# Optimization experiments

Measured on AMD Instinct MI355X. Metric: run time of the kernel, lower is better.

## Reference

```python
import jax, jax.numpy as jnp
import numpy as np
from jax import lax

NHEAD = 8
LAYER_POOL = [1, 3, 5]
NUM_KEYS = [2, 2, 2]
N_LAYERS = 6


def ln(x, w, b, eps=1e-5):
    m = x.mean(-1, keepdims=True)
    v = ((x - m) ** 2).mean(-1, keepdims=True)
    return (x - m) / jnp.sqrt(v + eps) * w + b


def separable_attn(x, Wt, bt, Ws, bs_, Wo, bo, B, t, wh, pool_k):
    # x: (L, B, C), L = 1 + t*wh. Separable temporal->spatial attention with
    # std-based temporal token selection (VidTR compact pooling).
    L, _, C = x.shape
    hd = C // NHEAD
    scale = hd ** -0.5
    qkv = x @ Wt + bt                               # (L,B,3C)
    q, k_, v = jnp.split(qkv, 3, axis=-1)
    # --- cls token: full attention over all L tokens ---
    qc = (q[:1] * scale).reshape(1, B, NHEAD, hd)
    kf = k_.reshape(L, B, NHEAD, hd)
    vf = v.reshape(L, B, NHEAD, hd)
    ac = jax.nn.softmax(jnp.einsum('qbhd,lbhd->bhql', qc, kf), axis=-1)
    cls_out = jnp.einsum('bhql,lbhd->qbhd', ac, vf).reshape(1, B, C)
    # --- temporal attention per spatial location ---
    def resh_t(a):
        return a[1:].reshape(t, wh, B, NHEAD, hd).transpose(3, 2, 1, 0, 4)  # (h,B,wh,t,hd)
    qt, kt, vt = resh_t(q) * scale, resh_t(k_), resh_t(v)
    at = jax.nn.softmax(jnp.einsum('hbwqd,hbwkd->hbwqk', qt, kt), axis=-1)  # (h,B,wh,t,t)
    if pool_k > 0:
        sigma = jnp.std(at, axis=-1, ddof=1)        # (h,B,wh,t) row-wise std of attn
        _, idx = lax.top_k(sigma, t - pool_k)        # keep t-k most informative frames
        idx = jnp.sort(idx, axis=-1)                 # restore temporal order
        at = jnp.take_along_axis(at, idx[..., None], axis=3)  # (h,B,wh,t',t)
    else:
        idx = None
    ot = jnp.einsum('hbwqk,hbwkd->hbwqd', at, vt)    # (h,B,wh,t',hd)
    tp = ot.shape[3]
    y = ot.transpose(3, 2, 1, 0, 4).reshape(tp, wh, B, C)
    # --- spatial attention per frame (separate projections) ---
    qkv_s = y @ Ws + bs_
    qs, ks, vs = jnp.split(qkv_s, 3, axis=-1)
    def resh_s(a):
        return a.reshape(tp, wh, B, NHEAD, hd).transpose(3, 2, 0, 1, 4)  # (h,B,t',wh,hd)
    qs, ks, vs = resh_s(qs) * scale, resh_s(ks), resh_s(vs)
    as_ = jax.nn.softmax(jnp.einsum('hbtqd,hbtkd->hbtqk', qs, ks), axis=-1)
    os_ = jnp.einsum('hbtqk,hbtkd->hbtqd', as_, vs)  # (h,B,t',wh,hd)
    y = os_.transpose(2, 3, 1, 0, 4).reshape(tp * wh, B, C)
    out = jnp.concatenate([cls_out, y], axis=0) @ Wo + bo
    return out, idx


def pool_residual(src, idx, B, t, wh):
    # Gather-based temporal pooling of the residual path (the headroom target).
    C = src.shape[-1]
    hd = C // NHEAD
    cls_tok = src[:1]
    twh = src[1:].reshape(t, wh, B, NHEAD, hd).transpose(3, 2, 1, 0, 4)  # (h,B,wh,t,hd)
    twh = jnp.take_along_axis(twh, idx[..., None], axis=3)               # (h,B,wh,t',hd)
    tp = idx.shape[-1]
    twh = twh.transpose(3, 2, 1, 0, 4).reshape(tp * wh, B, C)
    return jnp.concatenate([cls_tok, twh], axis=0)


def setup_inputs() -> dict:
    key = jax.random.key(0)
    ks = jax.random.split(key, 12)
    C, F, ncls, t, P, B = 512, 2048, 157, 16, 16, 8
    def rn(k, shp, s=0.02):
        return jax.random.normal(k, shp, jnp.float32) * s
    return {
        'src': jax.random.normal(ks[0], (B, 3, t, 224, 224), jnp.float32),
        'conv_w': rn(ks[1], (C, 3, 1, P, P)),
        'conv_b': jnp.zeros((C,), jnp.float32),
        'cls_tok': rn(ks[2], (1, 1, C)),
        'pos': rn(ks[3], (1, t * 14 * 14 + 1, C)),
        'Wt': rn(ks[4], (N_LAYERS, C, 3 * C)), 'bt': jnp.zeros((N_LAYERS, 3 * C), jnp.float32),
        'Ws': rn(ks[5], (N_LAYERS, C, 3 * C)), 'bs_': jnp.zeros((N_LAYERS, 3 * C), jnp.float32),
        'Wo': rn(ks[6], (N_LAYERS, C, C)), 'bo': jnp.zeros((N_LAYERS, C), jnp.float32),
        'n1w': jnp.ones((N_LAYERS, C), jnp.float32), 'n1b': jnp.zeros((N_LAYERS, C), jnp.float32),
        'n2w': jnp.ones((N_LAYERS, C), jnp.float32), 'n2b': jnp.zeros((N_LAYERS, C), jnp.float32),
        'W1': rn(ks[7], (N_LAYERS, C, F)), 'b1': jnp.zeros((N_LAYERS, F), jnp.float32),
        'W2': rn(ks[8], (N_LAYERS, F, C)), 'b2': jnp.zeros((N_LAYERS, C), jnp.float32),
        'enw': jnp.ones((C,), jnp.float32), 'enb': jnp.zeros((C,), jnp.float32),
        'fcw': rn(ks[9], (C, ncls)), 'fcb': jnp.zeros((ncls,), jnp.float32),
    }


def reference(src, conv_w, conv_b, cls_tok, pos, Wt, bt, Ws, bs_, Wo, bo,
              n1w, n1b, n2w, n2b, W1, b1, W2, b2, enw, enb, fcw, fcb):
    B = src.shape[0]
    x = lax.conv_general_dilated(src, conv_w, window_strides=(1, 16, 16), padding='VALID',
                                 dimension_numbers=('NCDHW', 'OIDHW', 'NCDHW'))
    x = x + conv_b[None, :, None, None, None]      # (B,C,t,14,14)
    _, C, t, h, w = x.shape
    wh = h * w
    x = x.reshape(B, C, t * wh).transpose(2, 0, 1)  # (t*wh, B, C)
    x = jnp.concatenate([jnp.broadcast_to(cls_tok.transpose(1, 0, 2), (1, B, C)), x], axis=0)
    pos_e = pos.transpose(1, 0, 2)                  # (L,1,C), broadcasts over B
    for i in range(N_LAYERS):
        src2 = ln(x, n1w[i], n1b[i])
        qin = src2 + pos_e if i == 0 else src2
        pk = NUM_KEYS[LAYER_POOL.index(i)] if i in LAYER_POOL else 0
        attn_out, idx = separable_attn(qin, Wt[i], bt[i], Ws[i], bs_[i], Wo[i], bo[i], B, t, wh, pk)
        if i in LAYER_POOL:
            x = pool_residual(x, idx, B, t, wh)
            t = t - pk
        x = x + attn_out
        src2 = ln(x, n2w[i], n2b[i])
        x = x + jax.nn.relu(src2 @ W1[i] + b1[i]) @ W2[i] + b2[i]
    x = ln(x, enw, enb)
    return x[0] @ fcw + fcb                          # (B, activity_num)
```

## Files before the change

### kernel.cpp

```cpp
#include <hip/hip_runtime.h>
#include <math.h>


#define BB 8
#define CC 512
#define HH 8
#define HD 64
#define WHT 196
#define NCLS 157
#define CA_NCH 32

typedef short bf16x8 __attribute__((ext_vector_type(8)));
typedef float floatx4 __attribute__((ext_vector_type(4)));

__device__ __forceinline__ unsigned short f2bf(float f) {
  unsigned u = __float_as_uint(f);
  unsigned r = u + 0x7FFFu + ((u >> 16) & 1u);
  return (unsigned short)(r >> 16);
}
__device__ __forceinline__ float bf2f(unsigned short h) {
  return __uint_as_float((unsigned)h << 16);
}
__device__ __forceinline__ void splitf(float x, unsigned short& h, unsigned short& l) {
  unsigned u = __float_as_uint(x);
  unsigned hs = u >> 16;
  float rem = x - __uint_as_float(hs << 16);
  h = (unsigned short)hs;
  l = f2bf(rem);
}

__device__ __forceinline__ void glds16(const unsigned short* g, unsigned short* l) {
  __builtin_amdgcn_global_load_lds(
      (const __attribute__((address_space(1))) void*)g,
      (__attribute__((address_space(3))) void*)l, 16, 0, 0);
}

__device__ __forceinline__ float wave_reduce_sum(float v) {
#pragma unroll
  for (int o = 32; o > 0; o >>= 1) v += __shfl_down(v, o, 64);
  return v;
}
__device__ __forceinline__ float wave_reduce_max(float v) {
#pragma unroll
  for (int o = 32; o > 0; o >>= 1) v = fmaxf(v, __shfl_down(v, o, 64));
  return v;
}

__device__ __forceinline__ void xcd_decode(int id, int G, int nt,
                                           int& m0, int& n0) {
  int q8 = G >> 3, r8 = G & 7;
  int xcd = id & 7, j = id >> 3;
  int w = (xcd < r8) ? xcd * (q8 + 1) + j : r8 * (q8 + 1) + (xcd - r8) * q8 + j;
  m0 = (w / nt) * 128;
  n0 = (w % nt) * 128;
}

__global__ __launch_bounds__(256)
void im2col_split_kernel(const float* __restrict__ src,
                         unsigned short* __restrict__ IMhi,
                         unsigned short* __restrict__ IMlo) {
  int gid = blockIdx.x * 256 + threadIdx.x;
  int k4 = gid % 192;
  int u = gid / 192;
  if (u >= 25088) return;
  int b = u & 7;
  int s = u >> 3;
  int tt = s / WHT;
  int w2 = s % WHT;
  int ph = w2 / 14, pw = w2 % 14;
  int k = k4 * 4;
  int ci = k >> 8;
  int rem = k & 255;
  int py = rem >> 4, px = rem & 15;
  const float* sp = src + (size_t)b * (3 * 16 * 224 * 224) +
                    (size_t)ci * (16 * 224 * 224) + (size_t)tt * (224 * 224) +
                    (size_t)(ph * 16 + py) * 224 + pw * 16 + px;
  float4 v = *(const float4*)sp;
  ushort4 h, l;
  splitf(v.x, h.x, l.x);
  splitf(v.y, h.y, l.y);
  splitf(v.z, h.z, l.z);
  splitf(v.w, h.w, l.w);
  *(ushort4*)(IMhi + (size_t)u * 768 + k) = h;
  *(ushort4*)(IMlo + (size_t)u * 768 + k) = l;
}

__global__ __launch_bounds__(256)
void wsplit_flat_kernel(const float* __restrict__ W,
                        unsigned short* __restrict__ Whi,
                        unsigned short* __restrict__ Wlo, int total) {
  int i = blockIdx.x * 256 + threadIdx.x;
  if (i >= total) return;
  float w = W[i];
  unsigned short hi = f2bf(w);
  Whi[i] = hi;
  Wlo[i] = f2bf(w - bf2f(hi));
}

__global__ void cls_init_kernel(const float* __restrict__ clst, float* __restrict__ X) {
  X[(size_t)blockIdx.x * CC + threadIdx.x] = clst[threadIdx.x];
}

__global__ void copy_cls_kernel(const float* __restrict__ cls,
                                unsigned short* __restrict__ A) {
  A[(size_t)blockIdx.x * CC + threadIdx.x] =
      f2bf(cls[(size_t)blockIdx.x * CC + threadIdx.x]);
}

__global__ __launch_bounds__(256)
void ln_bf16_kernel(const float* __restrict__ X, unsigned short* __restrict__ O,
                    const float* __restrict__ w, const float* __restrict__ b) {
  __shared__ float red[8];
  const int row = blockIdx.x, tid = threadIdx.x;
  const float* x = X + (size_t)row * CC;
  float v0 = x[tid], v1 = x[tid + 256];
  float s = wave_reduce_sum(v0 + v1);
  if ((tid & 63) == 0) red[tid >> 6] = s;
  __syncthreads();
  float mean = (red[0] + red[1] + red[2] + red[3]) * (1.f / 512.f);
  float d0 = v0 - mean, d1 = v1 - mean;
  float vs = wave_reduce_sum(d0 * d0 + d1 * d1);
  if ((tid & 63) == 0) red[4 + (tid >> 6)] = vs;
  __syncthreads();
  float var = (red[4] + red[5] + red[6] + red[7]) * (1.f / 512.f);
  float inv = 1.0f / sqrtf(var + 1e-5f);
  O[(size_t)row * CC + tid] = f2bf(d0 * inv * w[tid] + b[tid]);
  O[(size_t)row * CC + tid + 256] = f2bf(d1 * inv * w[tid + 256] + b[tid + 256]);
}

__global__ __launch_bounds__(256)
void ln_split_kernel(const float* __restrict__ X,
                     unsigned short* __restrict__ Ahi,
                     unsigned short* __restrict__ Alo,
                     const float* __restrict__ w, const float* __restrict__ b,
                     const float* __restrict__ pos) {
  __shared__ float red[8];
  const int row = blockIdx.x, tid = threadIdx.x;
  const float* x = X + (size_t)row * CC;
  float v0 = x[tid], v1 = x[tid + 256];
  float s = wave_reduce_sum(v0 + v1);
  if ((tid & 63) == 0) red[tid >> 6] = s;
  __syncthreads();
  float mean = (red[0] + red[1] + red[2] + red[3]) * (1.f / 512.f);
  float d0 = v0 - mean, d1 = v1 - mean;
  float vs = wave_reduce_sum(d0 * d0 + d1 * d1);
  if ((tid & 63) == 0) red[4 + (tid >> 6)] = vs;
  __syncthreads();
  float var = (red[4] + red[5] + red[6] + red[7]) * (1.f / 512.f);
  float inv = 1.0f / sqrtf(var + 1e-5f);
  float o0 = d0 * inv * w[tid] + b[tid];
  float o1 = d1 * inv * w[tid + 256] + b[tid + 256];
  if (pos) {
    const float* pr = pos + (size_t)(row >> 3) * CC;
    o0 += pr[tid];
    o1 += pr[tid + 256];
  }
  unsigned short h, l;
  splitf(o0, h, l);
  Ahi[(size_t)row * CC + tid] = h;
  Alo[(size_t)row * CC + tid] = l;
  splitf(o1, h, l);
  Ahi[(size_t)row * CC + tid + 256] = h;
  Alo[(size_t)row * CC + tid + 256] = l;
}

__global__ __launch_bounds__(256)
void wtrans_kernel(const float* __restrict__ W, unsigned short* __restrict__ WT,
                   int N, int K) {
  __shared__ float tile[32][33];
  const int tid = threadIdx.x;
  const int tx = tid & 31, ty = tid >> 5;
  const int n0 = blockIdx.x * 32, k0 = blockIdx.y * 32;
#pragma unroll
  for (int r = 0; r < 4; r++) {
    int kk = ty + r * 8;
    tile[kk][tx] = W[(size_t)(k0 + kk) * N + n0 + tx];
  }
  __syncthreads();
#pragma unroll
  for (int r = 0; r < 4; r++) {
    int nn = ty + r * 8;
    WT[(size_t)(n0 + nn) * K + k0 + tx] = f2bf(tile[tx][nn]);
  }
}

__global__ __launch_bounds__(256)
void wtrans_split_kernel(const float* __restrict__ W,
                         unsigned short* __restrict__ WThi,
                         unsigned short* __restrict__ WTlo, int N, int K) {
  __shared__ float tile[32][33];
  const int tid = threadIdx.x;
  const int tx = tid & 31, ty = tid >> 5;
  const int n0 = blockIdx.x * 32, k0 = blockIdx.y * 32;
#pragma unroll
  for (int r = 0; r < 4; r++) {
    int kk = ty + r * 8;
    tile[kk][tx] = W[(size_t)(k0 + kk) * N + n0 + tx];
  }
  __syncthreads();
#pragma unroll
  for (int r = 0; r < 4; r++) {
    int nn = ty + r * 8;
    float w = tile[tx][nn];
    unsigned short hi = f2bf(w);
    unsigned short lo = f2bf(w - bf2f(hi));
    WThi[(size_t)(n0 + nn) * K + k0 + tx] = hi;
    WTlo[(size_t)(n0 + nn) * K + k0 + tx] = lo;
  }
}

template <int RELU, int RES, int OBF>
__global__ __launch_bounds__(256)
void mfma_gemm_kernel(const unsigned short* __restrict__ A,
                      const unsigned short* __restrict__ WT,
                      const float* __restrict__ bias, void* __restrict__ Cout,
                      int M, int N, int K, const float* __restrict__ resid) {
  __shared__ __attribute__((aligned(16))) unsigned short As[128 * 64];
  __shared__ __attribute__((aligned(16))) unsigned short Bs[128 * 64];
  const int tid = threadIdx.x;
  const int wave = tid >> 6, lane = tid & 63;
  const int quad = lane >> 4, l16 = lane & 15;
  const int wrow = (wave >> 1) * 64, wcol = (wave & 1) * 64;
  int m0, n0;
  xcd_decode(blockIdx.x, gridDim.x, N >> 7, m0, n0);

  floatx4 acc[4][4];
#pragma unroll
  for (int i = 0; i < 4; i++)
#pragma unroll
    for (int j = 0; j < 4; j++) acc[i][j] = (floatx4){0.f, 0.f, 0.f, 0.f};

  for (int k0 = 0; k0 < K; k0 += 64) {
#pragma unroll
    for (int t = 0; t < 4; t++) {
      int rl = wave * 32 + t * 8 + (lane >> 3);
      int g = (lane & 7) ^ (rl & 7);
      glds16(A + (size_t)(m0 + rl) * K + k0 + g * 8, &As[(wave * 32 + t * 8) * 64]);
      glds16(WT + (size_t)(n0 + rl) * K + k0 + g * 8, &Bs[(wave * 32 + t * 8) * 64]);
    }
    __syncthreads();
#pragma unroll
    for (int st = 0; st < 2; st++) {
      bf16x8 af[4], bf[4];
#pragma unroll
      for (int i = 0; i < 4; i++) {
        int ra = wrow + i * 16 + l16;
        af[i] = *(const bf16x8*)&As[ra * 64 + (((st * 4 + quad) ^ (ra & 7)) * 8)];
        int rb = wcol + i * 16 + l16;
        bf[i] = *(const bf16x8*)&Bs[rb * 64 + (((st * 4 + quad) ^ (rb & 7)) * 8)];
      }
#pragma unroll
      for (int i = 0; i < 4; i++)
#pragma unroll
        for (int j = 0; j < 4; j++)
          acc[i][j] = __builtin_amdgcn_mfma_f32_16x16x32_bf16(af[i], bf[j],
                                                              acc[i][j], 0, 0, 0);
    }
    __syncthreads();
  }
#pragma unroll
  for (int i = 0; i < 4; i++) {
#pragma unroll
    for (int p = 0; p < 4; p++) {
      int gm = m0 + wrow + i * 16 + quad * 4 + p;
      if (gm >= M) continue;
#pragma unroll
      for (int j = 0; j < 4; j++) {
        int gn = n0 + wcol + j * 16 + l16;
        float v = acc[i][j][p] + bias[gn];
        if (RELU) v = fmaxf(v, 0.f);
        if (RES == 1) v += resid[(size_t)gm * N + gn];
        if (OBF)
          ((unsigned short*)Cout)[(size_t)gm * N + gn] = f2bf(v);
        else
          ((float*)Cout)[(size_t)gm * N + gn] = v;
      }
    }
  }
}

__global__ __launch_bounds__(256)
void mfma_gemm3s_kernel(const unsigned short* __restrict__ Ahi,
                        const unsigned short* __restrict__ Alo,
                        const unsigned short* __restrict__ WThi,
                        const unsigned short* __restrict__ WTlo,
                        const float* __restrict__ bias, float* __restrict__ Cout,
                        int M, int N, int K) {
  __shared__ __attribute__((aligned(16))) unsigned short AsHi[128 * 32];
  __shared__ __attribute__((aligned(16))) unsigned short AsLo[128 * 32];
  __shared__ __attribute__((aligned(16))) unsigned short BsHi[128 * 32];
  __shared__ __attribute__((aligned(16))) unsigned short BsLo[128 * 32];
  const int tid = threadIdx.x;
  const int wave = tid >> 6, lane = tid & 63;
  const int quad = lane >> 4, l16 = lane & 15;
  const int wrow = (wave >> 1) * 64, wcol = (wave & 1) * 64;
  int m0, n0;
  xcd_decode(blockIdx.x, gridDim.x, N >> 7, m0, n0);

  floatx4 acc[4][4];
#pragma unroll
  for (int i = 0; i < 4; i++)
#pragma unroll
    for (int j = 0; j < 4; j++) acc[i][j] = (floatx4){0.f, 0.f, 0.f, 0.f};

  for (int k0 = 0; k0 < K; k0 += 32) {
#pragma unroll
    for (int t = 0; t < 2; t++) {
      int rl = wave * 32 + t * 16 + (lane >> 2);
      int g = (lane & 3) ^ ((rl >> 1) & 3);
      size_t soff = (size_t)(m0 + rl) * K + k0 + g * 8;
      size_t boff = (size_t)(n0 + rl) * K + k0 + g * 8;
      unsigned short* lb = (unsigned short*)0 + (wave * 32 + t * 16) * 32;
      glds16(Ahi + soff, &AsHi[(wave * 32 + t * 16) * 32]);
      glds16(Alo + soff, &AsLo[(wave * 32 + t * 16) * 32]);
      glds16(WThi + boff, &BsHi[(wave * 32 + t * 16) * 32]);
      glds16(WTlo + boff, &BsLo[(wave * 32 + t * 16) * 32]);
      (void)lb;
    }
    __syncthreads();
    bf16x8 ah[4], al[4], bh[4], bl[4];
#pragma unroll
    for (int i = 0; i < 4; i++) {
      int ra = wrow + i * 16 + l16;
      int offa = ra * 32 + ((quad ^ ((ra >> 1) & 3)) * 8);
      ah[i] = *(const bf16x8*)&AsHi[offa];
      al[i] = *(const bf16x8*)&AsLo[offa];
      int rb = wcol + i * 16 + l16;
      int offb = rb * 32 + ((quad ^ ((rb >> 1) & 3)) * 8);
      bh[i] = *(const bf16x8*)&BsHi[offb];
      bl[i] = *(const bf16x8*)&BsLo[offb];
    }
#pragma unroll
    for (int i = 0; i < 4; i++)
#pragma unroll
      for (int j = 0; j < 4; j++) {
        acc[i][j] = __builtin_amdgcn_mfma_f32_16x16x32_bf16(ah[i], bh[j],
                                                            acc[i][j], 0, 0, 0);
        acc[i][j] = __builtin_amdgcn_mfma_f32_16x16x32_bf16(ah[i], bl[j],
                                                            acc[i][j], 0, 0, 0);
        acc[i][j] = __builtin_amdgcn_mfma_f32_16x16x32_bf16(al[i], bh[j],
                                                            acc[i][j], 0, 0, 0);
      }
    __syncthreads();
  }
#pragma unroll
  for (int i = 0; i < 4; i++) {
#pragma unroll
    for (int p = 0; p < 4; p++) {
      int gm = m0 + wrow + i * 16 + quad * 4 + p;
      if (gm >= M) continue;
#pragma unroll
      for (int j = 0; j < 4; j++) {
        int gn = n0 + wcol + j * 16 + l16;
        Cout[(size_t)gm * N + gn] = acc[i][j][p] + bias[gn];
      }
    }
  }
}

__global__ __launch_bounds__(256)
void class_attn_part_kernel(const float* __restrict__ qkv,
                            float* __restrict__ part, int L) {
  __shared__ float q[64];
  __shared__ float sc[128];
  __shared__ float red[8];
  __shared__ float pv[256];
  const int h = blockIdx.x & 7, b = blockIdx.x >> 3;
  const int chunk = blockIdx.y;
  const int tid = threadIdx.x;
  const int per = (L + CA_NCH - 1) / CA_NCH;
  const int l0 = chunk * per;
  const int nl = min(L - l0, per);
  if (tid < 64) q[tid] = qkv[(size_t)b * 1536 + h * 64 + tid] * 0.125f;
  __syncthreads();
  float lmax = -3.4e38f;
  for (int i = tid; i < nl; i += 256) {
    const float* kr = qkv + (size_t)((l0 + i) * 8 + b) * 1536 + 512 + h * 64;
    float s = 0;
#pragma unroll
    for (int d2 = 0; d2 < 64; d2 += 4) {
      float4 k4 = *(const float4*)(kr + d2);
      s += q[d2] * k4.x + q[d2 + 1] * k4.y + q[d2 + 2] * k4.z + q[d2 + 3] * k4.w;
    }
    sc[i] = s;
    lmax = fmaxf(lmax, s);
  }
  lmax = wave_reduce_max(lmax);
  if ((tid & 63) == 0) red[tid >> 6] = lmax;
  __syncthreads();
  float gmax = fmaxf(fmaxf(red[0], red[1]), fmaxf(red[2], red[3]));
  float lsum = 0;
  for (int i = tid; i < nl; i += 256) {
    float e = expf(sc[i] - gmax);
    sc[i] = e;
    lsum += e;
  }
  lsum = wave_reduce_sum(lsum);
  if ((tid & 63) == 0) red[4 + (tid >> 6)] = lsum;
  __syncthreads();
  float gsum = red[4] + red[5] + red[6] + red[7];
  const int g = tid >> 6, d = tid & 63;
  float acc = 0;
  for (int i = g; i < nl; i += 4)
    acc += sc[i] * qkv[(size_t)((l0 + i) * 8 + b) * 1536 + 1024 + h * 64 + d];
  pv[g * 64 + d] = acc;
  __syncthreads();
  float* rec = part + ((size_t)blockIdx.x * CA_NCH + chunk) * 68;
  if (tid == 0) {
    rec[0] = gmax;
    rec[1] = gsum;
  }
  if (g == 0) rec[2 + d] = pv[d] + pv[64 + d] + pv[128 + d] + pv[192 + d];
}

__global__ __launch_bounds__(64)
void class_attn_reduce_kernel(const float* __restrict__ part,
                              float* __restrict__ cls) {
  const int hb = blockIdx.x;
  const int tid = threadIdx.x;
  const float* prec = part + (size_t)hb * CA_NCH * 68;
  float M = -3.4e38f;
#pragma unroll
  for (int c = 0; c < CA_NCH; c++) M = fmaxf(M, prec[c * 68]);
  float total = 0.f, acc = 0.f;
#pragma unroll
  for (int c = 0; c < CA_NCH; c++) {
    float w = expf(prec[c * 68] - M);
    total += prec[c * 68 + 1] * w;
    acc += prec[c * 68 + 2 + tid] * w;
  }
  int h = hb & 7, b = hb >> 3;
  cls[b * CC + h * 64 + tid] = acc / total;
}

__global__ __launch_bounds__(256)
void temporal_attn_kernel(const float* __restrict__ qkv,
                          unsigned short* __restrict__ Y,
                          int* __restrict__ idxbuf, int t, int tp, int pk) {
  __shared__ float qs[16 * 65], ks[16 * 65], vs[16 * 65];
  __shared__ float a[16 * 17];
  __shared__ float sig[16];
  __shared__ int keepf[16];
  __shared__ int klist[16];
  const int g = blockIdx.x;
  const int w = g % WHT;
  const int bb = (g / WHT) & 7;
  const int h = g / (WHT * 8);
  const int tid = threadIdx.x;
  const int td = t * 64;
  for (int e = tid; e < td; e += 256) {
    int tt = e >> 6, d = e & 63;
    size_t rb = (size_t)((1 + tt * WHT + w) * 8 + bb) * 1536 + h * 64 + d;
    qs[tt * 65 + d] = qkv[rb] * 0.125f;
    ks[tt * 65 + d] = qkv[rb + 512];
    vs[tt * 65 + d] = qkv[rb + 1024];
  }
  __syncthreads();
  if (tid < t * t) {
    int qi = tid / t, ki = tid % t;
    const float* qp = &qs[qi * 65];
    const float* kp = &ks[ki * 65];
    float s = 0;
#pragma unroll 8
    for (int d2 = 0; d2 < 64; d2++) s += qp[d2] * kp[d2];
    a[qi * 17 + ki] = s;
  }
  __syncthreads();
  if (tid < t) {
    float* row = &a[tid * 17];
    float m = row[0];
    for (int k2 = 1; k2 < t; k2++) m = fmaxf(m, row[k2]);
    float sum = 0;
    for (int k2 = 0; k2 < t; k2++) {
      float e2 = expf(row[k2] - m);
      row[k2] = e2;
      sum += e2;
    }
    float inv = 1.f / sum;
    for (int k2 = 0; k2 < t; k2++) row[k2] *= inv;
  }
  __syncthreads();
  if (pk > 0) {
    if (tid < t) {
      const float* row = &a[tid * 17];
      float mean = 0;
      for (int k2 = 0; k2 < t; k2++) mean += row[k2];
      mean /= (float)t;
      float var = 0;
      for (int k2 = 0; k2 < t; k2++) {
        float dl = row[k2] - mean;
        var += dl * dl;
      }
      var /= (float)(t - 1);
      sig[tid] = sqrtf(var);
    }
    __syncthreads();
    if (tid < t) {
      float sv = sig[tid];
      int r = 0;
      for (int q2 = 0; q2 < t; q2++) {
        float so = sig[q2];
        if (so > sv || (so == sv && q2 < tid)) r++;
      }
      keepf[tid] = (r < tp) ? 1 : 0;
    }
    __syncthreads();
    if (tid < t && keepf[tid]) {
      int ppos = 0;
      for (int q2 = 0; q2 < tid; q2++) ppos += keepf[q2];
      klist[ppos] = tid;
      idxbuf[((h * 8 + bb) * WHT + w) * 16 + ppos] = tid;
    }
  } else {
    if (tid < t) klist[tid] = tid;
  }
  __syncthreads();
  const int gq = tid >> 6, d = tid & 63;
  for (int qi = gq; qi < tp; qi += 4) {
    int qq = klist[qi];
    const float* arow = &a[qq * 17];
    float acc = 0;
    for (int k2 = 0; k2 < t; k2++) acc += arow[k2] * vs[k2 * 65 + d];
    Y[(size_t)((qi * WHT + w) * 8 + bb) * CC + h * 64 + d] = f2bf(acc);
  }
}

__global__ __launch_bounds__(256)
void pool_inplace_kernel(float* __restrict__ X, const int* __restrict__ idxbuf,
                         int tp) {
  const int b = blockIdx.x & 7;
  const int w = blockIdx.x >> 3;
  const int tid = threadIdx.x;
  const int c0 = tid, c1 = tid + 256;
  const int h0 = c0 >> 6, h1 = c1 >> 6;
  const int ib0 = ((h0 * 8 + b) * WHT + w) * 16;
  const int ib1 = ((h1 * 8 + b) * WHT + w) * 16;
  for (int q = 0; q < tp; q++) {
    int s0 = idxbuf[ib0 + q];
    int s1 = idxbuf[ib1 + q];
    size_t drow = (size_t)((1 + q * WHT + w) * 8 + b) * CC;
    if (s0 != q) {
      size_t srow = (size_t)((1 + s0 * WHT + w) * 8 + b) * CC;
      X[drow + c0] = X[srow + c0];
    }
    if (s1 != q) {
      size_t srow = (size_t)((1 + s1 * WHT + w) * 8 + b) * CC;
      X[drow + c1] = X[srow + c1];
    }
  }
}

__global__ __launch_bounds__(256)
void spatial_mfma_kernel(const float* __restrict__ qkv,
                         unsigned short* __restrict__ outA) {
  __shared__ unsigned short Khi[208 * 72];
  __shared__ unsigned short Klo[208 * 72];
  __shared__ unsigned short Vthi[64 * 200];
  __shared__ unsigned short Vtlo[64 * 200];
  __shared__ unsigned int Ps[4][16 * 196];
  const int blk = blockIdx.x;
  const int h = blk & 7;
  const int b = (blk >> 3) & 7;
  const int tq = blk >> 6;
  const int tid = threadIdx.x;
  const int wave = tid >> 6, lane = tid & 63;
  const int quad = lane >> 4, l16 = lane & 15;
  const size_t rowbase = (size_t)(tq * WHT) * 8 + b;

  union BF8 { bf16x8 v; unsigned short s[8]; unsigned int u[4]; };

  for (int r = tid >> 4; r < WHT; r += 16) {
    int c = (tid & 15) * 4;
    const float* gk = qkv + (rowbase + (size_t)r * 8) * 1536 + 512 + h * 64 + c;
    float4 kv = *(const float4*)gk;
    ushort4 khs, kls;
    splitf(kv.x, khs.x, kls.x);
    splitf(kv.y, khs.y, kls.y);
    splitf(kv.z, khs.z, kls.z);
    splitf(kv.w, khs.w, kls.w);
    *(ushort4*)&Khi[r * 72 + c] = khs;
    *(ushort4*)&Klo[r * 72 + c] = kls;
    const float* gv = qkv + (rowbase + (size_t)r * 8) * 1536 + 1024 + h * 64 + c;
    float4 vv = *(const float4*)gv;
    unsigned short vh, vl;
    splitf(vv.x, vh, vl); Vthi[(c + 0) * 200 + r] = vh; Vtlo[(c + 0) * 200 + r] = vl;
    splitf(vv.y, vh, vl); Vthi[(c + 1) * 200 + r] = vh; Vtlo[(c + 1) * 200 + r] = vl;
    splitf(vv.z, vh, vl); Vthi[(c + 2) * 200 + r] = vh; Vtlo[(c + 2) * 200 + r] = vl;
    splitf(vv.w, vh, vl); Vthi[(c + 3) * 200 + r] = vh; Vtlo[(c + 3) * 200 + r] = vl;
  }
  __syncthreads();

  unsigned int* myP = &Ps[wave][0];

  for (int strip = wave; strip < 13; strip += 4) {
    int qr = strip * 16 + l16;
    int qrc = min(qr, WHT - 1);
    const float* qp = qkv + (rowbase + (size_t)qrc * 8) * 1536 + h * 64 + quad * 8;
    BF8 qh[2], ql[2];
#pragma unroll
    for (int st = 0; st < 2; st++) {
      float4 a = *(const float4*)(qp + st * 32);
      float4 c = *(const float4*)(qp + st * 32 + 4);
      float vals[8] = {a.x, a.y, a.z, a.w, c.x, c.y, c.z, c.w};
#pragma unroll
      for (int i = 0; i < 8; i++) {
        float x = vals[i] * 0.125f;
        splitf(x, qh[st].s[i], ql[st].s[i]);
      }
    }

    floatx4 acc_s[13];
#pragma unroll
    for (int j = 0; j < 13; j++) {
      floatx4 acc = (floatx4){0.f, 0.f, 0.f, 0.f};
#pragma unroll
      for (int st = 0; st < 2; st++) {
        bf16x8 bh = *(const bf16x8*)&Khi[(j * 16 + l16) * 72 + st * 32 + quad * 8];
        bf16x8 bl = *(const bf16x8*)&Klo[(j * 16 + l16) * 72 + st * 32 + quad * 8];
        acc = __builtin_amdgcn_mfma_f32_16x16x32_bf16(qh[st].v, bh, acc, 0, 0, 0);
        acc = __builtin_amdgcn_mfma_f32_16x16x32_bf16(ql[st].v, bh, acc, 0, 0, 0);
        acc = __builtin_amdgcn_mfma_f32_16x16x32_bf16(qh[st].v, bl, acc, 0, 0, 0);
      }
      acc_s[j] = acc;
    }
    if (l16 >= 4) acc_s[12] = (floatx4){-3.4e38f, -3.4e38f, -3.4e38f, -3.4e38f};

    float inv4[4];
#pragma unroll
    for (int p = 0; p < 4; p++) {
      float m = acc_s[0][p];
#pragma unroll
      for (int j = 1; j < 13; j++) m = fmaxf(m, acc_s[j][p]);
#pragma unroll
      for (int o = 8; o >= 1; o >>= 1) m = fmaxf(m, __shfl_xor(m, o, 64));
      float s = 0.f;
#pragma unroll
      for (int j = 0; j < 13; j++) {
        float e = __expf(acc_s[j][p] - m);
        acc_s[j][p] = e;
        s += e;
      }
#pragma unroll
      for (int o = 8; o >= 1; o >>= 1) s += __shfl_xor(s, o, 64);
      inv4[p] = 1.f / s;
    }

#pragma unroll
    for (int j = 0; j < 12; j++) {
#pragma unroll
      for (int p = 0; p < 4; p++) {
        float e = acc_s[j][p];
        unsigned u = __float_as_uint(e);
        unsigned hs = u >> 16;
        float rem = e - __uint_as_float(hs << 16);
        unsigned ls = f2bf(rem);
        myP[(quad * 4 + p) * 196 + j * 16 + l16] = hs | (ls << 16);
      }
    }

    floatx4 acc_o[4];
#pragma unroll
    for (int jn = 0; jn < 4; jn++) acc_o[jn] = (floatx4){0.f, 0.f, 0.f, 0.f};
#pragma unroll
    for (int s = 0; s < 6; s++) {
      const unsigned int* pp = &myP[l16 * 196 + s * 32 + quad * 8];
      uint4 u0 = *(const uint4*)pp;
      uint4 u1 = *(const uint4*)(pp + 4);
      BF8 AH, AL;
      AH.u[0] = (u0.x & 0xffffu) | (u0.y << 16);
      AH.u[1] = (u0.z & 0xffffu) | (u0.w << 16);
      AH.u[2] = (u1.x & 0xffffu) | (u1.y << 16);
      AH.u[3] = (u1.z & 0xffffu) | (u1.w << 16);
      AL.u[0] = (u0.x >> 16) | (u0.y & 0xffff0000u);
      AL.u[1] = (u0.z >> 16) | (u0.w & 0xffff0000u);
      AL.u[2] = (u1.x >> 16) | (u1.y & 0xffff0000u);
      AL.u[3] = (u1.z >> 16) | (u1.w & 0xffff0000u);
#pragma unroll
      for (int jn = 0; jn < 4; jn++) {
        bf16x8 bh = *(const bf16x8*)&Vthi[(jn * 16 + l16) * 200 + s * 32 + quad * 8];
        bf16x8 bl = *(const bf16x8*)&Vtlo[(jn * 16 + l16) * 200 + s * 32 + quad * 8];
        acc_o[jn] = __builtin_amdgcn_mfma_f32_16x16x32_bf16(AH.v, bh, acc_o[jn], 0, 0, 0);
        acc_o[jn] = __builtin_amdgcn_mfma_f32_16x16x32_bf16(AL.v, bh, acc_o[jn], 0, 0, 0);
        acc_o[jn] = __builtin_amdgcn_mfma_f32_16x16x32_bf16(AH.v, bl, acc_o[jn], 0, 0, 0);
      }
    }
#pragma unroll
    for (int kk = 0; kk < 4; kk++) {
      int srcl = (lane & 48) + kk;
      float e0 = __shfl(acc_s[12][0], srcl, 64);
      float e1 = __shfl(acc_s[12][1], srcl, 64);
      float e2 = __shfl(acc_s[12][2], srcl, 64);
      float e3 = __shfl(acc_s[12][3], srcl, 64);
#pragma unroll
      for (int jn = 0; jn < 4; jn++) {
        int d = jn * 16 + l16;
        float v = bf2f(Vthi[d * 200 + 192 + kk]) + bf2f(Vtlo[d * 200 + 192 + kk]);
        acc_o[jn][0] += e0 * v;
        acc_o[jn][1] += e1 * v;
        acc_o[jn][2] += e2 * v;
        acc_o[jn][3] += e3 * v;
      }
    }

#pragma unroll
    for (int jn = 0; jn < 4; jn++) {
#pragma unroll
      for (int p = 0; p < 4; p++) {
        int qrow = strip * 16 + quad * 4 + p;
        if (qrow < WHT)
          outA[((size_t)(1 + tq * WHT + qrow) * 8 + b) * CC + h * 64 + jn * 16 + l16] =
              f2bf(acc_o[jn][p] * inv4[p]);
      }
    }
  }
}

__global__ __launch_bounds__(256)
void head_kernel(const float* __restrict__ X, const float* __restrict__ enw,
                 const float* __restrict__ enb, const float* __restrict__ fcw,
                 const float* __restrict__ fcb, float* __restrict__ out) {
  __shared__ float nx[512];
  __shared__ float red[8];
  const int b = blockIdx.x, tid = threadIdx.x;
  const float* x = X + (size_t)b * CC;
  float v0 = x[tid], v1 = x[tid + 256];
  float s = wave_reduce_sum(v0 + v1);
  if ((tid & 63) == 0) red[tid >> 6] = s;
  __syncthreads();
  float mean = (red[0] + red[1] + red[2] + red[3]) * (1.f / 512.f);
  float d0 = v0 - mean, d1 = v1 - mean;
  float vs = wave_reduce_sum(d0 * d0 + d1 * d1);
  if ((tid & 63) == 0) red[4 + (tid >> 6)] = vs;
  __syncthreads();
  float var = (red[4] + red[5] + red[6] + red[7]) * (1.f / 512.f);
  float inv = 1.0f / sqrtf(var + 1e-5f);
  nx[tid] = d0 * inv * enw[tid] + enb[tid];
  nx[tid + 256] = d1 * inv * enw[tid + 256] + enb[tid + 256];
  __syncthreads();
  if (tid < NCLS) {
    float acc = fcb[tid];
    for (int c = 0; c < 512; c++) acc += nx[c] * fcw[c * NCLS + tid];
    out[b * NCLS + tid] = acc;
  }
}

extern "C" void kernel_launch(void* const* d_in, const int* in_sizes, int n_in,
                              void* d_out, int out_size, void* d_ws, size_t ws_size,
                              hipStream_t stream) {
  (void)in_sizes; (void)n_in; (void)out_size; (void)ws_size;
  const float* src  = (const float*)d_in[0];
  const float* cw   = (const float*)d_in[1];
  const float* cb   = (const float*)d_in[2];
  const float* clst = (const float*)d_in[3];
  const float* pos  = (const float*)d_in[4];
  const float* Wt   = (const float*)d_in[5];
  const float* bt   = (const float*)d_in[6];
  const float* Wsp  = (const float*)d_in[7];
  const float* bsp  = (const float*)d_in[8];
  const float* Wo   = (const float*)d_in[9];
  const float* bo   = (const float*)d_in[10];
  const float* n1w  = (const float*)d_in[11];
  const float* n1b  = (const float*)d_in[12];
  const float* n2w  = (const float*)d_in[13];
  const float* n2b  = (const float*)d_in[14];
  const float* W1   = (const float*)d_in[15];
  const float* b1   = (const float*)d_in[16];
  const float* W2   = (const float*)d_in[17];
  const float* b2   = (const float*)d_in[18];
  const float* enw  = (const float*)d_in[19];
  const float* enb  = (const float*)d_in[20];
  const float* fcw  = (const float*)d_in[21];
  const float* fcb  = (const float*)d_in[22];

  float* ws = (float*)d_ws;
  const size_t TOKR = (size_t)3137 * 8;
  float* X0  = ws;
  float* Ab  = X0 + TOKR * 512;
  float* QKV = Ab + TOKR * 512;
  float* CLS = QKV + TOKR * 1536;
  int*   IDX = (int*)(CLS + 8 * 512);
  unsigned short* WT1 = (unsigned short*)(IDX + 8 * 8 * WHT * 16);
  unsigned short* WT2 = WT1 + 2048 * 512;
  float* PART = (float*)(WT2 + 2048 * 512);

  unsigned short* Ahi = (unsigned short*)Ab;
  unsigned short* Alo = Ahi + TOKR * 512;
  unsigned short* Abf = (unsigned short*)Ab;
  unsigned short* MIDb = (unsigned short*)QKV;
  unsigned short* IMhi = (unsigned short*)QKV;
  unsigned short* IMlo = IMhi + (size_t)25088 * 768;

  wsplit_flat_kernel<<<(512 * 768 + 255) / 256, 256, 0, stream>>>(
      cw, WT1, WT2, 512 * 768);
  im2col_split_kernel<<<(25088 * 192) / 256, 256, 0, stream>>>(src, IMhi, IMlo);
  mfma_gemm3s_kernel<<<(25088 / 128) * 4, 256, 0, stream>>>(
      IMhi, IMlo, WT1, WT2, cb, X0 + 8 * CC, 25088, 512, 768);
  cls_init_kernel<<<8, 512, 0, stream>>>(clst, X0);

  float* Xc = X0;
  int t = 16;
  const int FFN_CHUNK = 16384;
  for (int i = 0; i < 6; i++) {
    const int pk = (i & 1) ? 2 : 0;
    const int tp = t - pk;
    const int L = 1 + t * WHT;
    const int Lo = 1 + tp * WHT;
    const int M = L * 8, Mo = Lo * 8, My = tp * WHT * 8;
    const int mtM = (M + 127) / 128, mtMo = (Mo + 127) / 128, mtMy = (My + 127) / 128;

    ln_split_kernel<<<M, 256, 0, stream>>>(Xc, Ahi, Alo,
                                           n1w + (size_t)i * 512, n1b + (size_t)i * 512,
                                           (i == 0) ? pos : nullptr);
    wtrans_split_kernel<<<dim3(1536 / 32, 512 / 32), 256, 0, stream>>>(
        Wt + (size_t)i * 512 * 1536, WT1, WT2, 1536, 512);
    mfma_gemm3s_kernel<<<mtM * 12, 256, 0, stream>>>(
        Ahi, Alo, WT1, WT2, bt + (size_t)i * 1536, QKV, M, 1536, 512);
    class_attn_part_kernel<<<dim3(64, CA_NCH), 256, 0, stream>>>(QKV, PART, L);
    class_attn_reduce_kernel<<<64, 64, 0, stream>>>(PART, CLS);
    temporal_attn_kernel<<<HH * BB * WHT, 256, 0, stream>>>(QKV, Abf, IDX, t, tp, pk);
    wtrans_kernel<<<dim3(1536 / 32, 512 / 32), 256, 0, stream>>>(
        Wsp + (size_t)i * 512 * 1536, WT1, 1536, 512);
    mfma_gemm_kernel<0, 0, 0><<<mtMy * 12, 256, 0, stream>>>(
        Abf, WT1, bsp + (size_t)i * 1536, QKV, My, 1536, 512, nullptr);
    copy_cls_kernel<<<8, 512, 0, stream>>>(CLS, Abf);
    spatial_mfma_kernel<<<64 * tp, 256, 0, stream>>>(QKV, Abf);
    if (pk > 0)
      pool_inplace_kernel<<<8 * WHT, 256, 0, stream>>>(Xc, IDX, tp);
    wtrans_kernel<<<dim3(512 / 32, 512 / 32), 256, 0, stream>>>(
        Wo + (size_t)i * 512 * 512, WT1, 512, 512);
    mfma_gemm_kernel<0, 1, 0><<<mtMo * 4, 256, 0, stream>>>(
        Abf, WT1, bo + (size_t)i * 512, Xc, Mo, 512, 512, Xc);
    ln_bf16_kernel<<<Mo, 256, 0, stream>>>(Xc, Abf, n2w + (size_t)i * 512,
                                           n2b + (size_t)i * 512);
    wtrans_kernel<<<dim3(2048 / 32, 512 / 32), 256, 0, stream>>>(
        W1 + (size_t)i * 512 * 2048, WT1, 2048, 512);
    wtrans_kernel<<<dim3(512 / 32, 2048 / 32), 256, 0, stream>>>(
        W2 + (size_t)i * 2048 * 512, WT2, 512, 2048);
    for (int off = 0; off < Mo; off += FFN_CHUNK) {
      int R = Mo - off;
      if (R > FFN_CHUNK) R = FFN_CHUNK;
      int mtR = (R + 127) / 128;
      mfma_gemm_kernel<1, 0, 1><<<mtR * 16, 256, 0, stream>>>(
          Abf + (size_t)off * 512, WT1, b1 + (size_t)i * 2048,
          MIDb + (size_t)off * 2048, R, 2048, 512, nullptr);
      mfma_gemm_kernel<0, 1, 0><<<mtR * 4, 256, 0, stream>>>(
          MIDb + (size_t)off * 2048, WT2, b2 + (size_t)i * 512,
          Xc + (size_t)off * 512, R, 512, 2048, Xc + (size_t)off * 512);
    }
    t = tp;
  }
  head_kernel<<<8, 256, 0, stream>>>(Xc, enw, enb, fcw, fcb, (float*)d_out);
}
```

Measured before the change: 4.001 ms.

## Double-buffer LDS tiles in both MFMA GEMM kernels to overlap loads with compute

Result: no change. 4.075 ms (+1.9%).

```diff
diff --git a/kernel.cpp b/kernel.cpp
--- a/kernel.cpp
+++ b/kernel.cpp
@@ -215,8 +215,8 @@
                       const unsigned short* __restrict__ WT,
                       const float* __restrict__ bias, void* __restrict__ Cout,
                       int M, int N, int K, const float* __restrict__ resid) {
-  __shared__ __attribute__((aligned(16))) unsigned short As[128 * 64];
-  __shared__ __attribute__((aligned(16))) unsigned short Bs[128 * 64];
+  __shared__ __attribute__((aligned(16))) unsigned short As[2][128 * 32];
+  __shared__ __attribute__((aligned(16))) unsigned short Bs[2][128 * 32];
   const int tid = threadIdx.x;
   const int wave = tid >> 6, lane = tid & 63;
   const int quad = lane >> 4, l16 = lane & 15;
@@ -224,39 +224,54 @@
   int m0, n0;
   xcd_decode(blockIdx.x, gridDim.x, N >> 7, m0, n0);
 
+  const int rl0 = wave * 32 + (lane >> 2);
+  const int gg = lane & 3;
+
   floatx4 acc[4][4];
 #pragma unroll
   for (int i = 0; i < 4; i++)
 #pragma unroll
     for (int j = 0; j < 4; j++) acc[i][j] = (floatx4){0.f, 0.f, 0.f, 0.f};
 
-  for (int k0 = 0; k0 < K; k0 += 64) {
-#pragma unroll
-    for (int t = 0; t < 4; t++) {
-      int rl = wave * 32 + t * 8 + (lane >> 3);
-      int g = (lane & 7) ^ (rl & 7);
-      glds16(A + (size_t)(m0 + rl) * K + k0 + g * 8, &As[(wave * 32 + t * 8) * 64]);
-      glds16(WT + (size_t)(n0 + rl) * K + k0 + g * 8, &Bs[(wave * 32 + t * 8) * 64]);
-    }
+  const int nt = K >> 5;
+#pragma unroll
+  for (int t = 0; t < 2; t++) {
+    int rl = rl0 + t * 16;
+    int g = gg ^ ((rl >> 1) & 3);
+    glds16(A + (size_t)(m0 + rl) * K + g * 8, &As[0][(wave * 32 + t * 16) * 32]);
+    glds16(WT + (size_t)(n0 + rl) * K + g * 8, &Bs[0][(wave * 32 + t * 16) * 32]);
+  }
+  __syncthreads();
+  int buf = 0;
+  for (int it = 0; it < nt; ++it) {
+    if (it + 1 < nt) {
+      int k1 = (it + 1) << 5;
+#pragma unroll
+      for (int t = 0; t < 2; t++) {
+        int rl = rl0 + t * 16;
+        int g = gg ^ ((rl >> 1) & 3);
+        glds16(A + (size_t)(m0 + rl) * K + k1 + g * 8,
+               &As[buf ^ 1][(wave * 32 + t * 16) * 32]);
+        glds16(WT + (size_t)(n0 + rl) * K + k1 + g * 8,
+               &Bs[buf ^ 1][(wave * 32 + t * 16) * 32]);
+      }
+    }
+    bf16x8 af[4], bf[4];
+#pragma unroll
+    for (int i = 0; i < 4; i++) {
+      int ra = wrow + i * 16 + l16;
+      af[i] = *(const bf16x8*)&As[buf][ra * 32 + ((quad ^ ((ra >> 1) & 3)) * 8)];
+      int rb = wcol + i * 16 + l16;
+      bf[i] = *(const bf16x8*)&Bs[buf][rb * 32 + ((quad ^ ((rb >> 1) & 3)) * 8)];
+    }
+#pragma unroll
+    for (int i = 0; i < 4; i++)
+#pragma unroll
+      for (int j = 0; j < 4; j++)
+        acc[i][j] = __builtin_amdgcn_mfma_f32_16x16x32_bf16(af[i], bf[j],
+                                                            acc[i][j], 0, 0, 0);
     __syncthreads();
-#pragma unroll
-    for (int st = 0; st < 2; st++) {
-      bf16x8 af[4], bf[4];
-#pragma unroll
-      for (int i = 0; i < 4; i++) {
-        int ra = wrow + i * 16 + l16;
-        af[i] = *(const bf16x8*)&As[ra * 64 + (((st * 4 + quad) ^ (ra & 7)) * 8)];
-        int rb = wcol + i * 16 + l16;
-        bf[i] = *(const bf16x8*)&Bs[rb * 64 + (((st * 4 + quad) ^ (rb & 7)) * 8)];
-      }
-#pragma unroll
-      for (int i = 0; i < 4; i++)
-#pragma unroll
-        for (int j = 0; j < 4; j++)
-          acc[i][j] = __builtin_amdgcn_mfma_f32_16x16x32_bf16(af[i], bf[j],
-                                                              acc[i][j], 0, 0, 0);
-    }
-    __syncthreads();
+    buf ^= 1;
   }
 #pragma unroll
   for (int i = 0; i < 4; i++) {
@@ -286,10 +301,10 @@
                         const unsigned short* __restrict__ WTlo,
                         const float* __restrict__ bias, float* __restrict__ Cout,
                         int M, int N, int K) {
-  __shared__ __attribute__((aligned(16))) unsigned short AsHi[128 * 32];
-  __shared__ __attribute__((aligned(16))) unsigned short AsLo[128 * 32];
-  __shared__ __attribute__((aligned(16))) unsigned short BsHi[128 * 32];
-  __shared__ __attribute__((aligned(16))) unsigned short BsLo[128 * 32];
+  __shared__ __attribute__((aligned(16))) unsigned short AsHi[2][128 * 32];
+  __shared__ __attribute__((aligned(16))) unsigned short AsLo[2][128 * 32];
+  __shared__ __attribute__((aligned(16))) unsigned short BsHi[2][128 * 32];
+  __shared__ __attribute__((aligned(16))) unsigned short BsLo[2][128 * 32];
   const int tid = threadIdx.x;
   const int wave = tid >> 6, lane = tid & 63;
   const int quad = lane >> 4, l16 = lane & 15;
@@ -297,38 +312,57 @@
   int m0, n0;
   xcd_decode(blockIdx.x, gridDim.x, N >> 7, m0, n0);
 
+  const int rl0 = wave * 32 + (lane >> 2);
+  const int gg = lane & 3;
+
   floatx4 acc[4][4];
 #pragma unroll
   for (int i = 0; i < 4; i++)
 #pragma unroll
     for (int j = 0; j < 4; j++) acc[i][j] = (floatx4){0.f, 0.f, 0.f, 0.f};
 
-  for (int k0 = 0; k0 < K; k0 += 32) {
-#pragma unroll
-    for (int t = 0; t < 2; t++) {
-      int rl = wave * 32 + t * 16 + (lane >> 2);
-      int g = (lane & 3) ^ ((rl >> 1) & 3);
-      size_t soff = (size_t)(m0 + rl) * K + k0 + g * 8;
-      size_t boff = (size_t)(n0 + rl) * K + k0 + g * 8;
-      unsigned short* lb = (unsigned short*)0 + (wave * 32 + t * 16) * 32;
-      glds16(Ahi + soff, &AsHi[(wave * 32 + t * 16) * 32]);
-      glds16(Alo + soff, &AsLo[(wave * 32 + t * 16) * 32]);
-      glds16(WThi + boff, &BsHi[(wave * 32 + t * 16) * 32]);
-      glds16(WTlo + boff, &BsLo[(wave * 32 + t * 16) * 32]);
-      (void)lb;
-    }
-    __syncthreads();
+  const int nt = K >> 5;
+#pragma unroll
+  for (int t = 0; t < 2; t++) {
+    int rl = rl0 + t * 16;
+    int g = gg ^ ((rl >> 1) & 3);
+    size_t soff = (size_t)(m0 + rl) * K + g * 8;
+    size_t boff = (size_t)(n0 + rl) * K + g * 8;
+    int ldst = (wave * 32 + t * 16) * 32;
+    glds16(Ahi + soff, &AsHi[0][ldst]);
+    glds16(Alo + soff, &AsLo[0][ldst]);
+    glds16(WThi + boff, &BsHi[0][ldst]);
+    glds16(WTlo + boff, &BsLo[0][ldst]);
+  }
+  __syncthreads();
+  int buf = 0;
+  for (int it = 0; it < nt; ++it) {
+    if (it + 1 < nt) {
+      int k1 = (it + 1) << 5;
+#pragma unroll
+      for (int t = 0; t < 2; t++) {
+        int rl = rl0 + t * 16;
+        int g = gg ^ ((rl >> 1) & 3);
+        size_t soff = (size_t)(m0 + rl) * K + k1 + g * 8;
+        size_t boff = (size_t)(n0 + rl) * K + k1 + g * 8;
+        int ldst = (wave * 32 + t * 16) * 32;
+        glds16(Ahi + soff, &AsHi[buf ^ 1][ldst]);
+        glds16(Alo + soff, &AsLo[buf ^ 1][ldst]);
+        glds16(WThi + boff, &BsHi[buf ^ 1][ldst]);
+        glds16(WTlo + boff, &BsLo[buf ^ 1][ldst]);
+      }
+    }
     bf16x8 ah[4], al[4], bh[4], bl[4];
 #pragma unroll
     for (int i = 0; i < 4; i++) {
       int ra = wrow + i * 16 + l16;
       int offa = ra * 32 + ((quad ^ ((ra >> 1) & 3)) * 8);
-      ah[i] = *(const bf16x8*)&AsHi[offa];
-      al[i] = *(const bf16x8*)&AsLo[offa];
+      ah[i] = *(const bf16x8*)&AsHi[buf][offa];
+      al[i] = *(const bf16x8*)&AsLo[buf][offa];
       int rb = wcol + i * 16 + l16;
       int offb = rb * 32 + ((quad ^ ((rb >> 1) & 3)) * 8);
-      bh[i] = *(const bf16x8*)&BsHi[offb];
-      bl[i] = *(const bf16x8*)&BsLo[offb];
+      bh[i] = *(const bf16x8*)&BsHi[buf][offb];
+      bl[i] = *(const bf16x8*)&BsLo[buf][offb];
     }
 #pragma unroll
     for (int i = 0; i < 4; i++)
@@ -342,6 +376,7 @@
                                                             acc[i][j], 0, 0, 0);
       }
     __syncthreads();
+    buf ^= 1;
   }
 #pragma unroll
   for (int i = 0; i < 4; i++) {
```
